# Optimization experiments

Measured on AMD Instinct MI355X. Metric: run time of the kernel, lower is better.

Reference implementation:

```python
import jax, jax.numpy as jnp
import numpy as np

S = 2048
D = 2048
H = 16
HD = D // H
N_CHARS = 1024
LN_EPS = 1e-5


def setup_inputs() -> dict:
    key = jax.random.key(0)
    ks = jax.random.split(key, 12)
    byte_repr = jax.random.normal(ks[0], (S, D), dtype=jnp.float32)
    categories = jax.random.randint(ks[1], (S,), 0, 32, dtype=jnp.int32)
    case = jax.random.randint(ks[2], (S,), 0, 3, dtype=jnp.int32)
    combining = jax.random.randint(ks[3], (S,), 0, 2, dtype=jnp.int32)
    seg_ids = jnp.sort(jax.random.randint(ks[4], (S,), 0, N_CHARS, dtype=jnp.int32))
    sc = 0.02
    cat_emb = jax.random.normal(ks[5], (32, D), dtype=jnp.float32) * sc
    case_emb = jax.random.normal(ks[6], (3, D), dtype=jnp.float32) * sc
    comb_emb = jax.random.normal(ks[7], (2, D), dtype=jnp.float32) * sc
    ln_g = jnp.ones((D,), dtype=jnp.float32)
    ln_b = jnp.zeros((D,), dtype=jnp.float32)
    in_w = jax.random.normal(ks[8], (3 * D, D), dtype=jnp.float32) * (1.0 / np.sqrt(D))
    in_b = jnp.zeros((3 * D,), dtype=jnp.float32)
    out_w = jax.random.normal(ks[9], (D, D), dtype=jnp.float32) * (1.0 / np.sqrt(D))
    out_b = jnp.zeros((D,), dtype=jnp.float32)
    return {
        'byte_repr': byte_repr, 'categories': categories, 'case': case,
        'combining': combining, 'seg_ids': seg_ids,
        'cat_emb': cat_emb, 'case_emb': case_emb, 'comb_emb': comb_emb,
        'ln_g': ln_g, 'ln_b': ln_b,
        'in_w': in_w, 'in_b': in_b, 'out_w': out_w, 'out_b': out_b,
    }


def reference(byte_repr, categories, case, combining, seg_ids,
              cat_emb, case_emb, comb_emb, ln_g, ln_b,
              in_w, in_b, out_w, out_b):
    # fused embedding adds
    x = byte_repr + cat_emb[categories] + case_emb[case] + comb_emb[combining]
    # LayerNorm
    mu = jnp.mean(x, axis=-1, keepdims=True)
    var = jnp.mean(jnp.square(x - mu), axis=-1, keepdims=True)
    xn = (x - mu) * jax.lax.rsqrt(var + LN_EPS) * ln_g + ln_b
    # QKV projection (torch in_proj): [S, 3D]
    qkv = xn @ in_w.T + in_b
    q, k, v = jnp.split(qkv, 3, axis=-1)
    q = q.reshape(S, H, HD).transpose(1, 0, 2)  # [H,S,hd]
    k = k.reshape(S, H, HD).transpose(1, 0, 2)
    v = v.reshape(S, H, HD).transpose(1, 0, 2)
    # additive float mask: 1 inside a character block, 0 elsewhere
    mask = (seg_ids[:, None] == seg_ids[None, :]).astype(x.dtype)
    scores = jnp.einsum('hqd,hkd->hqk', q, k) / np.sqrt(HD) + mask[None]
    attn = jax.nn.softmax(scores, axis=-1)
    o = jnp.einsum('hqk,hkd->hqd', attn, v)  # [H,S,hd]
    o = o.transpose(1, 0, 2).reshape(S, D) @ out_w.T + out_b
    # residual; dropout is identity in eval
    return xn + o
```

## Files before the change

kernel.cpp:

```cpp
#include <hip/hip_runtime.h>
#include <hip/hip_bf16.h>

#define SS 2048
#define DD 2048
#define HH 16
#define HDIM 128

typedef unsigned short u16;
typedef __attribute__((ext_vector_type(8))) short bf16x8;
typedef __attribute__((ext_vector_type(4))) float f32x4;
typedef __attribute__((ext_vector_type(4))) unsigned short u16x4;

__device__ __forceinline__ u16 f2bf(float f){
  unsigned u = __float_as_uint(f);
  u += 0x7FFFu + ((u >> 16) & 1u);
  return (u16)(u >> 16);
}

__device__ __forceinline__ void gload_lds16(const void* g, void* l){
  __builtin_amdgcn_global_load_lds(
      (const __attribute__((address_space(1))) void*)g,
      (__attribute__((address_space(3))) void*)l, 16, 0, 0);
}

__device__ __forceinline__ f32x4 mfma16(bf16x8 a, bf16x8 b, f32x4 c){
  return __builtin_amdgcn_mfma_f32_16x16x32_bf16(a, b, c, 0, 0, 0);
}

__global__ __launch_bounds__(256) void k_embed_ln(
    const float* __restrict__ br, const int* __restrict__ cat,
    const int* __restrict__ cse, const int* __restrict__ cmb,
    const float* __restrict__ cat_e, const float* __restrict__ case_e,
    const float* __restrict__ comb_e, const float* __restrict__ lg,
    const float* __restrict__ lb, float* __restrict__ xn32, u16* __restrict__ xn16)
{
  const int s = blockIdx.x, t = threadIdx.x;
  const int lane = t & 63, wave = t >> 6;
  const int c0 = cat[s], c1 = cse[s], c2 = cmb[s];
  const f32x4* pb = (const f32x4*)(br + (size_t)s * DD);
  const f32x4* e0 = (const f32x4*)(cat_e + (size_t)c0 * DD);
  const f32x4* e1 = (const f32x4*)(case_e + (size_t)c1 * DD);
  const f32x4* e2 = (const f32x4*)(comb_e + (size_t)c2 * DD);
  f32x4 xa = pb[t] + e0[t] + e1[t] + e2[t];
  f32x4 xb = pb[t+256] + e0[t+256] + e1[t+256] + e2[t+256];
  float s1 = 0.f, s2 = 0.f;
#pragma unroll
  for (int i = 0; i < 4; ++i){ s1 += xa[i] + xb[i]; s2 += xa[i]*xa[i] + xb[i]*xb[i]; }
#pragma unroll
  for (int off = 32; off > 0; off >>= 1){ s1 += __shfl_down(s1, off); s2 += __shfl_down(s2, off); }
  __shared__ float red[8];
  if (lane == 0){ red[wave*2] = s1; red[wave*2+1] = s2; }
  __syncthreads();
  const float t1 = red[0]+red[2]+red[4]+red[6];
  const float t2 = red[1]+red[3]+red[5]+red[7];
  const float mean = t1 * (1.0f/DD);
  const float var  = t2 * (1.0f/DD) - mean*mean;
  const float rstd = rsqrtf(var + 1e-5f);
  const f32x4* g4 = (const f32x4*)lg;
  const f32x4* b4 = (const f32x4*)lb;
  f32x4 ga = g4[t], gb = g4[t+256], ba = b4[t], bb = b4[t+256];
  f32x4 ya, yb; u16x4 ha, hb;
#pragma unroll
  for (int i = 0; i < 4; ++i){
    ya[i] = (xa[i]-mean)*rstd*ga[i] + ba[i];
    yb[i] = (xb[i]-mean)*rstd*gb[i] + bb[i];
    ha[i] = f2bf(ya[i]); hb[i] = f2bf(yb[i]);
  }
  ((f32x4*)(xn32 + (size_t)s*DD))[t]     = ya;
  ((f32x4*)(xn32 + (size_t)s*DD))[t+256] = yb;
  ((u16x4*)(xn16 + (size_t)s*DD))[t]     = ha;
  ((u16x4*)(xn16 + (size_t)s*DD))[t+256] = hb;
}

__global__ __launch_bounds__(256) void k_f32_to_bf16(
    const float* __restrict__ in, u16* __restrict__ out, int n4)
{
  int i = blockIdx.x * blockDim.x + threadIdx.x;
  const int stride = gridDim.x * blockDim.x;
  for (; i < n4; i += stride){
    f32x4 v = ((const f32x4*)in)[i];
    u16x4 h;
#pragma unroll
    for (int j = 0; j < 4; ++j) h[j] = f2bf(v[j]);
    ((u16x4*)out)[i] = h;
  }
}

__device__ __forceinline__ void gemm_tile_128(
    const u16* A, const u16* B, int K, int bm, int bn,
    u16* lds_a, u16* lds_b, f32x4 acc[4][4])
{
  const int t = threadIdx.x;
  const int lane = t & 63;
  const int wm = (t >> 6) >> 1, wn = (t >> 6) & 1;
  const int g = lane >> 4, r16 = lane & 15;
  const u16* Ab = A + (size_t)bm * 128 * K;
  const u16* Bb = B + (size_t)bn * 128 * K;
  for (int kt = 0; kt < K; kt += 32){
#pragma unroll
    for (int half = 0; half < 2; ++half){
      const int tt = half*256 + t;
      const int row = tt >> 2, col = (tt & 3) * 8;
      gload_lds16(Ab + (size_t)row*K + kt + col, lds_a + tt*8);
      gload_lds16(Bb + (size_t)row*K + kt + col, lds_b + tt*8);
    }
    __syncthreads();
    bf16x8 af[4], bfr[4];
#pragma unroll
    for (int i = 0; i < 4; ++i){
      af[i]  = *(const bf16x8*)(lds_a + (wm*64 + i*16 + r16)*32 + g*8);
      bfr[i] = *(const bf16x8*)(lds_b + (wn*64 + i*16 + r16)*32 + g*8);
    }
#pragma unroll
    for (int a = 0; a < 4; ++a)
#pragma unroll
      for (int b = 0; b < 4; ++b)
        acc[a][b] = mfma16(af[a], bfr[b], acc[a][b]);
    __syncthreads();
  }
}

__global__ __launch_bounds__(256) void k_gemm_qkv(
    const u16* __restrict__ A, const u16* __restrict__ B, const float* __restrict__ bias,
    u16* __restrict__ qws, u16* __restrict__ kws, u16* __restrict__ vtws)
{
  __shared__ __align__(16) u16 lds_a[128*32];
  __shared__ __align__(16) u16 lds_b[128*32];
  const int bm = blockIdx.x, bn = blockIdx.y;
  f32x4 acc[4][4] = {};
  gemm_tile_128(A, B, DD, bm, bn, lds_a, lds_b, acc);
  const int t = threadIdx.x, lane = t & 63;
  const int wm = (t >> 6) >> 1, wn = (t >> 6) & 1;
  const int g = lane >> 4, r16 = lane & 15;
  const int which = bn >> 4, h = bn & 15;
  const float qscale = 0.08838834764831845f;
#pragma unroll
  for (int a = 0; a < 4; ++a){
#pragma unroll
    for (int b = 0; b < 4; ++b){
      const int hd = wn*64 + b*16 + r16;
      const float bi = bias[bn*128 + hd];
      const int s0 = bm*128 + wm*64 + a*16 + g*4;
      if (which == 0){
#pragma unroll
        for (int rr = 0; rr < 4; ++rr)
          qws[((size_t)h*SS + (s0+rr))*HDIM + hd] = f2bf((acc[a][b][rr] + bi) * qscale);
      } else if (which == 1){
#pragma unroll
        for (int rr = 0; rr < 4; ++rr)
          kws[((size_t)h*SS + (s0+rr))*HDIM + hd] = f2bf(acc[a][b][rr] + bi);
      } else {
        u16x4 pk;
#pragma unroll
        for (int rr = 0; rr < 4; ++rr) pk[rr] = f2bf(acc[a][b][rr] + bi);
        *(u16x4*)&vtws[((size_t)h*HDIM + hd)*SS + s0] = pk;
      }
    }
  }
}

__global__ __launch_bounds__(256) void k_attn(
    const u16* __restrict__ q, const u16* __restrict__ kk_, const u16* __restrict__ vt,
    const int* __restrict__ seg, u16* __restrict__ o)
{
  __shared__ __align__(16) u16 k_lds[64*136];
  __shared__ __align__(16) u16 v_lds[128*72];
  __shared__ __align__(16) u16 p_lds[4][16*72];
  __shared__ int seg_lds[64];
  const int qb = blockIdx.x, h = blockIdx.y;
  const int t = threadIdx.x, lane = t & 63, w = t >> 6;
  const int g = lane >> 4, r16 = lane & 15;

  bf16x8 qf[4];
  {
    const u16* qp = q + ((size_t)h*SS + qb*64 + w*16 + r16) * HDIM;
#pragma unroll
    for (int c = 0; c < 4; ++c) qf[c] = *(const bf16x8*)(qp + c*32 + g*8);
  }
  int sq[4];
#pragma unroll
  for (int rr = 0; rr < 4; ++rr) sq[rr] = seg[qb*64 + w*16 + g*4 + rr];

  f32x4 oacc[8] = {};
  float mrun[4], lrun[4];
#pragma unroll
  for (int rr = 0; rr < 4; ++rr){ mrun[rr] = -1e30f; lrun[rr] = 0.f; }

  for (int kt = 0; kt < 32; ++kt){
#pragma unroll
    for (int p4 = 0; p4 < 4; ++p4){
      const int tt = p4*256 + t;
      { const int row = tt >> 4, ch = tt & 15;
        *(bf16x8*)(k_lds + row*136 + ch*8) =
            *(const bf16x8*)(kk_ + ((size_t)h*SS + kt*64 + row)*HDIM + ch*8); }
      { const int row = tt >> 3, ch = tt & 7;
        *(bf16x8*)(v_lds + row*72 + ch*8) =
            *(const bf16x8*)(vt + ((size_t)h*HDIM + row)*SS + kt*64 + ch*8); }
    }
    if (t < 64) seg_lds[t] = seg[kt*64 + t];
    __syncthreads();

    f32x4 sacc[4] = {};
#pragma unroll
    for (int b = 0; b < 4; ++b)
#pragma unroll
      for (int c = 0; c < 4; ++c){
        bf16x8 kf = *(const bf16x8*)(k_lds + (b*16 + r16)*136 + c*32 + g*8);
        sacc[b] = mfma16(qf[c], kf, sacc[b]);
      }
#pragma unroll
    for (int b = 0; b < 4; ++b){
      const int sk = seg_lds[b*16 + r16];
#pragma unroll
      for (int rr = 0; rr < 4; ++rr)
        sacc[b][rr] += (sk == sq[rr]) ? 1.0f : 0.0f;
    }
    float mx[4];
#pragma unroll
    for (int rr = 0; rr < 4; ++rr)
      mx[rr] = fmaxf(fmaxf(sacc[0][rr], sacc[1][rr]), fmaxf(sacc[2][rr], sacc[3][rr]));
#pragma unroll
    for (int off = 8; off > 0; off >>= 1)
#pragma unroll
      for (int rr = 0; rr < 4; ++rr)
        mx[rr] = fmaxf(mx[rr], __shfl_xor(mx[rr], off));
    float mnew[4], sc[4], ps[4];
#pragma unroll
    for (int rr = 0; rr < 4; ++rr){
      mnew[rr] = fmaxf(mrun[rr], mx[rr]);
      sc[rr] = __expf(mrun[rr] - mnew[rr]);
      ps[rr] = 0.f;
    }
#pragma unroll
    for (int b = 0; b < 4; ++b)
#pragma unroll
      for (int rr = 0; rr < 4; ++rr){
        const float pv = __expf(sacc[b][rr] - mnew[rr]);
        sacc[b][rr] = pv;
        ps[rr] += pv;
      }
#pragma unroll
    for (int off = 8; off > 0; off >>= 1)
#pragma unroll
      for (int rr = 0; rr < 4; ++rr)
        ps[rr] += __shfl_xor(ps[rr], off);
#pragma unroll
    for (int rr = 0; rr < 4; ++rr){
      lrun[rr] = lrun[rr]*sc[rr] + ps[rr];
      mrun[rr] = mnew[rr];
    }
#pragma unroll
    for (int f = 0; f < 8; ++f)
#pragma unroll
      for (int rr = 0; rr < 4; ++rr)
        oacc[f][rr] *= sc[rr];
    u16* pw = p_lds[w];
#pragma unroll
    for (int b = 0; b < 4; ++b)
#pragma unroll
      for (int rr = 0; rr < 4; ++rr)
        pw[(g*4 + rr)*72 + b*16 + r16] = f2bf(sacc[b][rr]);
    __syncthreads();
#pragma unroll
    for (int c = 0; c < 2; ++c){
      bf16x8 pa = *(const bf16x8*)(pw + r16*72 + c*32 + g*8);
#pragma unroll
      for (int f = 0; f < 8; ++f){
        bf16x8 vf = *(const bf16x8*)(v_lds + (f*16 + r16)*72 + c*32 + g*8);
        oacc[f] = mfma16(pa, vf, oacc[f]);
      }
    }
    __syncthreads();
  }
#pragma unroll
  for (int f = 0; f < 8; ++f){
    const int hd = f*16 + r16;
#pragma unroll
    for (int rr = 0; rr < 4; ++rr){
      const int s = qb*64 + w*16 + g*4 + rr;
      o[(size_t)s*DD + h*HDIM + hd] = f2bf(oacc[f][rr] / lrun[rr]);
    }
  }
}

__global__ __launch_bounds__(256) void k_gemm_out(
    const u16* __restrict__ A, const u16* __restrict__ B, const float* __restrict__ bias,
    const float* __restrict__ xn32, float* __restrict__ out)
{
  __shared__ __align__(16) u16 lds_a[128*32];
  __shared__ __align__(16) u16 lds_b[128*32];
  const int bm = blockIdx.x, bn = blockIdx.y;
  f32x4 acc[4][4] = {};
  gemm_tile_128(A, B, DD, bm, bn, lds_a, lds_b, acc);
  const int t = threadIdx.x, lane = t & 63;
  const int wm = (t >> 6) >> 1, wn = (t >> 6) & 1;
  const int g = lane >> 4, r16 = lane & 15;
#pragma unroll
  for (int a = 0; a < 4; ++a){
#pragma unroll
    for (int b = 0; b < 4; ++b){
      const int n = bn*128 + wn*64 + b*16 + r16;
      const float bi = bias[n];
#pragma unroll
      for (int rr = 0; rr < 4; ++rr){
        const int s = bm*128 + wm*64 + a*16 + g*4 + rr;
        out[(size_t)s*DD + n] = acc[a][b][rr] + bi + xn32[(size_t)s*DD + n];
      }
    }
  }
}

extern "C" void kernel_launch(void* const* d_in, const int* in_sizes, int n_in,
                              void* d_out, int out_size, void* d_ws, size_t ws_size,
                              hipStream_t stream)
{
  (void)in_sizes; (void)n_in; (void)out_size; (void)ws_size;
  const float* br     = (const float*)d_in[0];
  const int*   cat    = (const int*)d_in[1];
  const int*   cse    = (const int*)d_in[2];
  const int*   cmb    = (const int*)d_in[3];
  const int*   seg    = (const int*)d_in[4];
  const float* cat_e  = (const float*)d_in[5];
  const float* case_e = (const float*)d_in[6];
  const float* comb_e = (const float*)d_in[7];
  const float* ln_g   = (const float*)d_in[8];
  const float* ln_b   = (const float*)d_in[9];
  const float* in_w   = (const float*)d_in[10];
  const float* in_b   = (const float*)d_in[11];
  const float* out_w  = (const float*)d_in[12];
  const float* out_b  = (const float*)d_in[13];
  float* out = (float*)d_out;

  char* ws = (char*)d_ws;
  float* xn32  = (float*)(ws);
  u16*   xn16  = (u16*)(ws + 16777216);
  u16*   inw16 = (u16*)(ws + 25165824);
  u16*   outw16= (u16*)(ws + 50331648);
  u16*   qws   = (u16*)(ws + 58720256);
  u16*   kws   = (u16*)(ws + 67108864);
  u16*   vtws  = (u16*)(ws + 75497472);
  u16*   ows   = (u16*)(ws + 83886080);

  k_embed_ln<<<SS, 256, 0, stream>>>(br, cat, cse, cmb, cat_e, case_e, comb_e,
                                     ln_g, ln_b, xn32, xn16);
  k_f32_to_bf16<<<2048, 256, 0, stream>>>(in_w, inw16, 3*DD*DD/4);
  k_f32_to_bf16<<<2048, 256, 0, stream>>>(out_w, outw16, DD*DD/4);
  dim3 g1(16, 48);
  k_gemm_qkv<<<g1, 256, 0, stream>>>(xn16, inw16, in_b, qws, kws, vtws);
  dim3 g2(32, 16);
  k_attn<<<g2, 256, 0, stream>>>(qws, kws, vtws, seg, ows);
  dim3 g3(16, 16);
  k_gemm_out<<<g3, 256, 0, stream>>>(ows, outw16, out_b, xn32, out);
}
```

Measured before the change: 370.3 us.

## Rewrite attention as split-K flash with 32x32 MFMA and register-only P

Restructures the attention kernel so each block handles 32 queries and its four waves split the key range, each running an independent online softmax. K and V are read straight from global memory into registers, with no LDS staging or per-tile barriers. P is rearranged between lanes with shuffles instead of going through LDS, and the partial results are merged across waves through LDS at the end. It also switches to 32x32x16 MFMA, skips rescaling while the running max grows by 8 or less, and doubles the grid. The cost is more global traffic because K and V are no longer shared across waves, plus higher register pressure.

```diff
diff --git a/kernel.cpp b/kernel.cpp
--- a/kernel.cpp
+++ b/kernel.cpp
@@ -9,7 +9,10 @@
 typedef unsigned short u16;
 typedef __attribute__((ext_vector_type(8))) short bf16x8;
 typedef __attribute__((ext_vector_type(4))) float f32x4;
+typedef __attribute__((ext_vector_type(16))) float f32x16;
 typedef __attribute__((ext_vector_type(4))) unsigned short u16x4;
+typedef __attribute__((ext_vector_type(4))) int i32x4;
+typedef __attribute__((ext_vector_type(4))) unsigned int u32x4;
 
 __device__ __forceinline__ u16 f2bf(float f){
   unsigned u = __float_as_uint(f);
@@ -25,6 +28,9 @@
 
 __device__ __forceinline__ f32x4 mfma16(bf16x8 a, bf16x8 b, f32x4 c){
   return __builtin_amdgcn_mfma_f32_16x16x32_bf16(a, b, c, 0, 0, 0);
+}
+__device__ __forceinline__ f32x16 mfma32(bf16x8 a, bf16x8 b, f32x16 c){
+  return __builtin_amdgcn_mfma_f32_32x32x16_bf16(a, b, c, 0, 0, 0);
 }
 
 __global__ __launch_bounds__(256) void k_embed_ln(
@@ -159,126 +165,138 @@
   }
 }
 
-__global__ __launch_bounds__(256) void k_attn(
+__global__ __launch_bounds__(256, 2) void k_attn(
     const u16* __restrict__ q, const u16* __restrict__ kk_, const u16* __restrict__ vt,
     const int* __restrict__ seg, u16* __restrict__ o)
 {
-  __shared__ __align__(16) u16 k_lds[64*136];
-  __shared__ __align__(16) u16 v_lds[128*72];
-  __shared__ __align__(16) u16 p_lds[4][16*72];
-  __shared__ int seg_lds[64];
+  __shared__ __align__(16) float obuf[4][4][32][36];
+  __shared__ float mlbuf[4][2][32];
   const int qb = blockIdx.x, h = blockIdx.y;
   const int t = threadIdx.x, lane = t & 63, w = t >> 6;
-  const int g = lane >> 4, r16 = lane & 15;
-
-  bf16x8 qf[4];
+  const int hi = lane >> 5, l31 = lane & 31;
+  const int q0 = qb * 32;
+
+  bf16x8 qf[8];
   {
-    const u16* qp = q + ((size_t)h*SS + qb*64 + w*16 + r16) * HDIM;
-#pragma unroll
-    for (int c = 0; c < 4; ++c) qf[c] = *(const bf16x8*)(qp + c*32 + g*8);
-  }
-  int sq[4];
-#pragma unroll
-  for (int rr = 0; rr < 4; ++rr) sq[rr] = seg[qb*64 + w*16 + g*4 + rr];
-
-  f32x4 oacc[8] = {};
-  float mrun[4], lrun[4];
-#pragma unroll
-  for (int rr = 0; rr < 4; ++rr){ mrun[rr] = -1e30f; lrun[rr] = 0.f; }
-
-  for (int kt = 0; kt < 32; ++kt){
-#pragma unroll
-    for (int p4 = 0; p4 < 4; ++p4){
-      const int tt = p4*256 + t;
-      { const int row = tt >> 4, ch = tt & 15;
-        *(bf16x8*)(k_lds + row*136 + ch*8) =
-            *(const bf16x8*)(kk_ + ((size_t)h*SS + kt*64 + row)*HDIM + ch*8); }
-      { const int row = tt >> 3, ch = tt & 7;
-        *(bf16x8*)(v_lds + row*72 + ch*8) =
-            *(const bf16x8*)(vt + ((size_t)h*HDIM + row)*SS + kt*64 + ch*8); }
-    }
-    if (t < 64) seg_lds[t] = seg[kt*64 + t];
-    __syncthreads();
-
-    f32x4 sacc[4] = {};
-#pragma unroll
-    for (int b = 0; b < 4; ++b)
-#pragma unroll
-      for (int c = 0; c < 4; ++c){
-        bf16x8 kf = *(const bf16x8*)(k_lds + (b*16 + r16)*136 + c*32 + g*8);
-        sacc[b] = mfma16(qf[c], kf, sacc[b]);
+    const u16* qp = q + ((size_t)h*SS + q0 + l31)*HDIM + hi*8;
+#pragma unroll
+    for (int c = 0; c < 8; ++c) qf[c] = *(const bf16x8*)(qp + c*16);
+  }
+  const int seg_q = seg[q0 + l31];
+
+  f32x16 oacc[4];
+#pragma unroll
+  for (int dg = 0; dg < 4; ++dg)
+#pragma unroll
+    for (int r = 0; r < 16; ++r) oacc[dg][r] = 0.f;
+  float m = -1e30f, l = 0.f;
+
+  const u16* kbase = kk_ + ((size_t)h*SS + l31)*HDIM + hi*8;
+  const u16* vbase = vt + ((size_t)h*HDIM + l31)*SS + hi*8;
+
+  for (int it = 0; it < 16; ++it){
+    const int kb = (w*16 + it)*32;
+    bf16x8 kf[8];
+    const u16* kp = kbase + (size_t)kb*HDIM;
+#pragma unroll
+    for (int c = 0; c < 8; ++c) kf[c] = *(const bf16x8*)(kp + c*16);
+    i32x4 sg[4];
+#pragma unroll
+    for (int rq = 0; rq < 4; ++rq) sg[rq] = *(const i32x4*)(seg + kb + rq*8 + hi*4);
+    bf16x8 vf[4][2];
+#pragma unroll
+    for (int dg = 0; dg < 4; ++dg)
+#pragma unroll
+      for (int ks = 0; ks < 2; ++ks)
+        vf[dg][ks] = *(const bf16x8*)(vbase + (size_t)dg*32*SS + kb + ks*16);
+
+    f32x16 s;
+#pragma unroll
+    for (int r = 0; r < 16; ++r) s[r] = 0.f;
+#pragma unroll
+    for (int c = 0; c < 8; ++c) s = mfma32(kf[c], qf[c], s);
+
+    float tm = -1e30f;
+#pragma unroll
+    for (int r = 0; r < 16; ++r){
+      const int sk = sg[r>>2][r&3];
+      s[r] += (sk == seg_q) ? 1.0f : 0.0f;
+      tm = fmaxf(tm, s[r]);
+    }
+    tm = fmaxf(tm, __shfl_xor(tm, 32));
+    if (!__all(tm <= m + 8.0f)){
+      const float mn = fmaxf(m, tm);
+      const float sc = __expf(m - mn);
+      l *= sc;
+#pragma unroll
+      for (int dg = 0; dg < 4; ++dg)
+#pragma unroll
+        for (int r = 0; r < 16; ++r) oacc[dg][r] *= sc;
+      m = mn;
+    }
+    float p[16]; float ts = 0.f;
+#pragma unroll
+    for (int r = 0; r < 16; ++r){ p[r] = __expf(s[r] - m); ts += p[r]; }
+    ts += __shfl_xor(ts, 32);
+    l += ts;
+    unsigned pk_[8];
+#pragma unroll
+    for (int i = 0; i < 8; ++i)
+      pk_[i] = (unsigned)f2bf(p[2*i]) | ((unsigned)f2bf(p[2*i+1]) << 16);
+    const unsigned x0 = __shfl_xor(hi ? pk_[0] : pk_[2], 32);
+    const unsigned x1 = __shfl_xor(hi ? pk_[1] : pk_[3], 32);
+    const unsigned x2 = __shfl_xor(hi ? pk_[4] : pk_[6], 32);
+    const unsigned x3 = __shfl_xor(hi ? pk_[5] : pk_[7], 32);
+    u32x4 f0, f1;
+    f0[0] = hi ? x0 : pk_[0]; f0[1] = hi ? x1 : pk_[1];
+    f0[2] = hi ? pk_[2] : x0; f0[3] = hi ? pk_[3] : x1;
+    f1[0] = hi ? x2 : pk_[4]; f1[1] = hi ? x3 : pk_[5];
+    f1[2] = hi ? pk_[6] : x2; f1[3] = hi ? pk_[7] : x3;
+    const bf16x8 pf0 = __builtin_bit_cast(bf16x8, f0);
+    const bf16x8 pf1 = __builtin_bit_cast(bf16x8, f1);
+#pragma unroll
+    for (int dg = 0; dg < 4; ++dg){
+      oacc[dg] = mfma32(vf[dg][0], pf0, oacc[dg]);
+      oacc[dg] = mfma32(vf[dg][1], pf1, oacc[dg]);
+    }
+  }
+
+#pragma unroll
+  for (int dg = 0; dg < 4; ++dg)
+#pragma unroll
+    for (int rq = 0; rq < 4; ++rq){
+      f32x4 v4;
+#pragma unroll
+      for (int j = 0; j < 4; ++j) v4[j] = oacc[dg][rq*4 + j];
+      *(f32x4*)&obuf[w][dg][l31][rq*8 + hi*4] = v4;
+    }
+  if (lane < 32){ mlbuf[w][0][l31] = m; mlbuf[w][1][l31] = l; }
+  __syncthreads();
+
+  {
+    const int dg = w;
+    float mw[4], lw[4];
+#pragma unroll
+    for (int wv = 0; wv < 4; ++wv){ mw[wv] = mlbuf[wv][0][l31]; lw[wv] = mlbuf[wv][1][l31]; }
+    const float mstar = fmaxf(fmaxf(mw[0],mw[1]), fmaxf(mw[2],mw[3]));
+    float cw[4]; float lstar = 0.f;
+#pragma unroll
+    for (int wv = 0; wv < 4; ++wv){ cw[wv] = __expf(mw[wv]-mstar); lstar += cw[wv]*lw[wv]; }
+    const float inv = 1.0f / lstar;
+#pragma unroll
+    for (int rq = 0; rq < 4; ++rq){
+      f32x4 a4 = {0.f,0.f,0.f,0.f};
+#pragma unroll
+      for (int wv = 0; wv < 4; ++wv){
+        const f32x4 v4 = *(const f32x4*)&obuf[wv][dg][l31][rq*8 + hi*4];
+#pragma unroll
+        for (int j = 0; j < 4; ++j) a4[j] += v4[j] * cw[wv];
       }
-#pragma unroll
-    for (int b = 0; b < 4; ++b){
-      const int sk = seg_lds[b*16 + r16];
-#pragma unroll
-      for (int rr = 0; rr < 4; ++rr)
-        sacc[b][rr] += (sk == sq[rr]) ? 1.0f : 0.0f;
-    }
-    float mx[4];
-#pragma unroll
-    for (int rr = 0; rr < 4; ++rr)
-      mx[rr] = fmaxf(fmaxf(sacc[0][rr], sacc[1][rr]), fmaxf(sacc[2][rr], sacc[3][rr]));
-#pragma unroll
-    for (int off = 8; off > 0; off >>= 1)
-#pragma unroll
-      for (int rr = 0; rr < 4; ++rr)
-        mx[rr] = fmaxf(mx[rr], __shfl_xor(mx[rr], off));
-    float mnew[4], sc[4], ps[4];
-#pragma unroll
-    for (int rr = 0; rr < 4; ++rr){
-      mnew[rr] = fmaxf(mrun[rr], mx[rr]);
-      sc[rr] = __expf(mrun[rr] - mnew[rr]);
-      ps[rr] = 0.f;
-    }
-#pragma unroll
-    for (int b = 0; b < 4; ++b)
-#pragma unroll
-      for (int rr = 0; rr < 4; ++rr){
-        const float pv = __expf(sacc[b][rr] - mnew[rr]);
-        sacc[b][rr] = pv;
-        ps[rr] += pv;
-      }
-#pragma unroll
-    for (int off = 8; off > 0; off >>= 1)
-#pragma unroll
-      for (int rr = 0; rr < 4; ++rr)
-        ps[rr] += __shfl_xor(ps[rr], off);
-#pragma unroll
-    for (int rr = 0; rr < 4; ++rr){
-      lrun[rr] = lrun[rr]*sc[rr] + ps[rr];
-      mrun[rr] = mnew[rr];
-    }
-#pragma unroll
-    for (int f = 0; f < 8; ++f)
-#pragma unroll
-      for (int rr = 0; rr < 4; ++rr)
-        oacc[f][rr] *= sc[rr];
-    u16* pw = p_lds[w];
-#pragma unroll
-    for (int b = 0; b < 4; ++b)
-#pragma unroll
-      for (int rr = 0; rr < 4; ++rr)
-        pw[(g*4 + rr)*72 + b*16 + r16] = f2bf(sacc[b][rr]);
-    __syncthreads();
-#pragma unroll
-    for (int c = 0; c < 2; ++c){
-      bf16x8 pa = *(const bf16x8*)(pw + r16*72 + c*32 + g*8);
-#pragma unroll
-      for (int f = 0; f < 8; ++f){
-        bf16x8 vf = *(const bf16x8*)(v_lds + (f*16 + r16)*72 + c*32 + g*8);
-        oacc[f] = mfma16(pa, vf, oacc[f]);
-      }
-    }
-    __syncthreads();
-  }
-#pragma unroll
-  for (int f = 0; f < 8; ++f){
-    const int hd = f*16 + r16;
-#pragma unroll
-    for (int rr = 0; rr < 4; ++rr){
-      const int s = qb*64 + w*16 + g*4 + rr;
-      o[(size_t)s*DD + h*HDIM + hd] = f2bf(oacc[f][rr] / lrun[rr]);
+      u16x4 h4;
+#pragma unroll
+      for (int j = 0; j < 4; ++j) h4[j] = f2bf(a4[j] * inv);
+      const int d0 = dg*32 + rq*8 + hi*4;
+      *(u16x4*)&o[((size_t)(q0 + l31))*DD + h*HDIM + d0] = h4;
     }
   }
 }
@@ -347,7 +365,7 @@
   k_f32_to_bf16<<<2048, 256, 0, stream>>>(out_w, outw16, DD*DD/4);
   dim3 g1(16, 48);
   k_gemm_qkv<<<g1, 256, 0, stream>>>(xn16, inw16, in_b, qws, kws, vtws);
-  dim3 g2(32, 16);
+  dim3 g2(64, 16);
   k_attn<<<g2, 256, 0, stream>>>(qws, kws, vtws, seg, ows);
   dim3 g3(16, 16);
   k_gemm_out<<<g3, 256, 0, stream>>>(ows, outw16, out_b, xn32, out);
```

Result: slower. 400.1 us (+8.1%).
